# Optimization experiments

Hardware: AMD Instinct MI355X
Metric: run time of the kernel (lower is better)

Reference implementation:

```python
import math
import jax, jax.numpy as jnp
import numpy as np

D_MODEL = 1024
D_HIDDEN = 4096
N_EXPERTS = 8
TOP_K = 2
CAPACITY_FACTOR = 1.25


def setup_inputs() -> dict:
    key = jax.random.key(0)
    ks = jax.random.split(key, 8)
    s = 0.02
    x = jax.random.normal(ks[0], (4, 2048, D_MODEL), dtype=jnp.float32)
    router_w = jax.random.normal(ks[1], (D_MODEL, N_EXPERTS), dtype=jnp.float32) * s
    router_b = jnp.zeros((N_EXPERTS,), dtype=jnp.float32)
    w1 = jax.random.normal(ks[2], (N_EXPERTS, D_MODEL, D_HIDDEN), dtype=jnp.float32) * s
    b1 = jnp.zeros((N_EXPERTS, D_HIDDEN), dtype=jnp.float32)
    w2 = jax.random.normal(ks[3], (N_EXPERTS, D_HIDDEN, D_MODEL), dtype=jnp.float32) * s
    b2 = jnp.zeros((N_EXPERTS, D_MODEL), dtype=jnp.float32)
    return {"x": x, "router_w": router_w, "router_b": router_b,
            "w1": w1, "b1": b1, "w2": w2, "b2": b2}


def reference(x, router_w, router_b, w1, b1, w2, b2):
    B, T, D = x.shape
    N = B * T
    E = N_EXPERTS
    capacity = max(1, math.ceil(N / E * CAPACITY_FACTOR))

    x_flat = x.reshape(N, D)
    # Router (torch casts input to float32 for router)
    logits = x_flat.astype(jnp.float32) @ router_w + router_b          # [N, E]
    gates = jax.nn.softmax(logits, axis=-1)                            # [N, E]

    _, topk_idx = jax.lax.top_k(gates, TOP_K)                          # [N, k]
    expert_mask = jax.nn.one_hot(topk_idx, E, dtype=jnp.int32).sum(1)  # [N, E]

    # Capacity masking via cumulative position per expert
    pos = jnp.cumsum(expert_mask, axis=0) - 1                          # [N, E]
    expert_mask = expert_mask * (pos < capacity)
    valid = expert_mask > 0                                            # [N, E] bool

    # Dispatch: scatter tokens into [E, capacity, D] buffers (invalid -> slot `capacity`)
    pos_c = jnp.where(valid, pos, capacity)                            # [N, E]
    e_idx = jnp.broadcast_to(jnp.arange(E), (N, E))
    dispatched = (x_flat[:, None, :] * valid[:, :, None].astype(x.dtype))
    buf = jnp.zeros((E, capacity + 1, D), x.dtype).at[
        e_idx.ravel(), pos_c.ravel()].add(dispatched.reshape(N * E, D))
    buf = buf[:, :capacity]                                            # [E, C, D]

    # Per-expert FFN as batched GEMMs (GELU exact, matching nn.GELU default)
    h = jax.nn.gelu(jnp.einsum('ecd,edh->ech', buf, w1) + b1[:, None, :],
                    approximate=False)
    out = jnp.einsum('ech,ehd->ecd', h, w2) + b2[:, None, :]           # [E, C, D]

    # Combine: gather each token's expert outputs, weight by raw softmax gate
    pos_g = jnp.minimum(pos_c, capacity - 1)
    gathered = out[e_idx, pos_g]                                       # [N, E, D]
    weights = (gates * valid).astype(x.dtype)                          # [N, E]
    y = jnp.einsum('ned,ne->nd', gathered, weights)
    return y.reshape(B, T, D)
```

## Files before the change

kernel.cpp:

```cpp
#include <hip/hip_runtime.h>
#include <math.h>

#define D_MODEL 1024
#define D_HIDDEN 4096
#define NEXP 8
#define NTOK 8192
#define CAP 1280

#define BM 128
#define BN 128
#define BK 32
#define KSPLIT 2
#define KHALF (D_HIDDEN / KSPLIT)

typedef __attribute__((ext_vector_type(8))) short short8x;
typedef __attribute__((ext_vector_type(4))) short short4x;
typedef __attribute__((ext_vector_type(4))) float float4x;

__device__ __forceinline__ short f2bf(float f) {
  unsigned u = __float_as_uint(f);
  unsigned r = (u + 0x7FFFu + ((u >> 16) & 1u)) >> 16;
  return (short)r;
}
__device__ __forceinline__ float bf2f(short s) {
  return __uint_as_float(((unsigned)(unsigned short)s) << 16);
}
__device__ __forceinline__ float gelu_fast(float v) {
  float u2 = v * (1.5957691216f + 0.0713548163f * v * v);
  return v / (1.0f + __expf(-u2));
}

#define GLDS16(g, l)                                                        \
  __builtin_amdgcn_global_load_lds(                                         \
      (const __attribute__((address_space(1))) void*)(g),                   \
      (__attribute__((address_space(3))) void*)(l), 16, 0, 0)

__global__ __launch_bounds__(256) void convert_x_kernel(
    const float* __restrict__ x, short* __restrict__ xbf) {
  size_t i = ((size_t)blockIdx.x * 256 + threadIdx.x) * 8;
  const float4* s = (const float4*)(x + i);
  float4 a = s[0], b = s[1];
  short8x o;
  o[0] = f2bf(a.x); o[1] = f2bf(a.y); o[2] = f2bf(a.z); o[3] = f2bf(a.w);
  o[4] = f2bf(b.x); o[5] = f2bf(b.y); o[6] = f2bf(b.z); o[7] = f2bf(b.w);
  *(short8x*)(xbf + i) = o;
}

__global__ __launch_bounds__(256) void transpose_kernel(
    const float* __restrict__ in, short* __restrict__ out, int K, int N) {
  __shared__ unsigned tile[32 * 65];
  int n0 = blockIdx.x * 64, k0 = blockIdx.y * 64, e = blockIdx.z;
  int t = threadIdx.x;
  int rr = t >> 4;
  int cc = (t & 15) * 4;
  const float* src = in + (size_t)e * K * N + (size_t)(k0 + rr) * N + n0 + cc;
  bool packer = (rr & 1) == 0;
  int mb = rr >> 1;
#pragma unroll
  for (int p = 0; p < 4; ++p) {
    float4 v = *(const float4*)(src + (size_t)p * 16 * N);
    float4 wv;
    wv.x = __shfl_xor(v.x, 16, 64);
    wv.y = __shfl_xor(v.y, 16, 64);
    wv.z = __shfl_xor(v.z, 16, 64);
    wv.w = __shfl_xor(v.w, 16, 64);
    if (packer) {
      int m = p * 8 + mb;
      unsigned* tr = &tile[m * 65 + cc];
      tr[0] = (unsigned)(unsigned short)f2bf(v.x) |
              ((unsigned)(unsigned short)f2bf(wv.x) << 16);
      tr[1] = (unsigned)(unsigned short)f2bf(v.y) |
              ((unsigned)(unsigned short)f2bf(wv.y) << 16);
      tr[2] = (unsigned)(unsigned short)f2bf(v.z) |
              ((unsigned)(unsigned short)f2bf(wv.z) << 16);
      tr[3] = (unsigned)(unsigned short)f2bf(v.w) |
              ((unsigned)(unsigned short)f2bf(wv.w) << 16);
    }
  }
  __syncthreads();
  int n = t >> 2, q = t & 3;
  const unsigned* col = &tile[q * 8 * 65 + n];
  unsigned d[8];
#pragma unroll
  for (int j = 0; j < 8; ++j) d[j] = col[j * 65];
  short* dst = out + (size_t)e * N * K + (size_t)(n0 + n) * K + k0 + q * 16;
  ((uint4*)dst)[0] = make_uint4(d[0], d[1], d[2], d[3]);
  ((uint4*)dst)[1] = make_uint4(d[4], d[5], d[6], d[7]);
}

__global__ __launch_bounds__(256) void router_kernel(
    const float* __restrict__ x, const float* __restrict__ rw,
    const float* __restrict__ rb, int2* __restrict__ tok_experts,
    float2* __restrict__ tok_gates) {
  int t = blockIdx.x * 4 + (threadIdx.x >> 6);
  int lane = threadIdx.x & 63;
  const float* xr = x + (size_t)t * D_MODEL;
  float acc[8];
#pragma unroll
  for (int e = 0; e < 8; ++e) acc[e] = 0.f;
#pragma unroll
  for (int kk = 0; kk < 16; ++kk) {
    int k = kk * 64 + lane;
    float xv = xr[k];
    const float4* wr = (const float4*)(rw + (size_t)k * 8);
    float4 w0 = wr[0], w1v = wr[1];
    acc[0] += xv * w0.x;  acc[1] += xv * w0.y;
    acc[2] += xv * w0.z;  acc[3] += xv * w0.w;
    acc[4] += xv * w1v.x; acc[5] += xv * w1v.y;
    acc[6] += xv * w1v.z; acc[7] += xv * w1v.w;
  }
#pragma unroll
  for (int off = 32; off > 0; off >>= 1) {
#pragma unroll
    for (int e = 0; e < 8; ++e) acc[e] += __shfl_xor(acc[e], off, 64);
  }
  if (lane == 0) {
    float lg[8];
#pragma unroll
    for (int e = 0; e < 8; ++e) lg[e] = acc[e] + rb[e];
    int e0 = 0;
#pragma unroll
    for (int e = 1; e < 8; ++e) if (lg[e] > lg[e0]) e0 = e;
    int e1 = (e0 == 0) ? 1 : 0;
#pragma unroll
    for (int e = 0; e < 8; ++e) if (e != e0 && lg[e] > lg[e1]) e1 = e;
    float mx = lg[e0];
    float s = 0.f;
#pragma unroll
    for (int e = 0; e < 8; ++e) s += expf(lg[e] - mx);
    float inv = 1.f / s;
    tok_experts[t] = make_int2(e0, e1);
    tok_gates[t] = make_float2(expf(lg[e0] - mx) * inv, expf(lg[e1] - mx) * inv);
  }
}

__global__ __launch_bounds__(1024) void scan_kernel(
    const int2* __restrict__ tok_experts, int* __restrict__ slot_token,
    int* __restrict__ token_rows) {
  int e = blockIdx.x;
  int tid = threadIdx.x;
  for (int i = tid; i < CAP; i += 1024) slot_token[e * CAP + i] = -1;
  __shared__ int wsum[16];
  __shared__ int running;
  if (tid == 0) running = 0;
  __syncthreads();
  int lane = tid & 63, wid = tid >> 6;
  unsigned long long lmask = (1ull << lane) - 1ull;
  for (int base = 0; base < NTOK; base += 1024) {
    int t = base + tid;
    int2 ee = tok_experts[t];
    int m = (ee.x == e || ee.y == e) ? 1 : 0;
    unsigned long long bal = __ballot(m);
    int prefix = __popcll(bal & lmask);
    if (lane == 0) wsum[wid] = (int)__popcll(bal);
    __syncthreads();
    if (tid == 0) {
      int s = running;
#pragma unroll
      for (int w = 0; w < 16; ++w) { int v = wsum[w]; wsum[w] = s; s += v; }
      running = s;
    }
    __syncthreads();
    if (m) {
      int pos = wsum[wid] + prefix;
      int which = (ee.x == e) ? 0 : 1;
      if (pos < CAP) {
        slot_token[e * CAP + pos] = t;
        token_rows[2 * t + which] = e * CAP + pos;
      } else {
        token_rows[2 * t + which] = -1;
      }
    }
    __syncthreads();
  }
}


__global__ __launch_bounds__(256) void gemm1_fast(
    const short* __restrict__ xbf, const short* __restrict__ w1t,
    const float* __restrict__ b1, const int* __restrict__ slot_token,
    short* __restrict__ h) {
  __shared__ short As[BM * BK];
  __shared__ short Bs[BN * BK];
  __shared__ int rowtok[BM];
  int bx = blockIdx.x;
  int e = bx & 7, ct = (bx >> 3) & 31, rt = bx >> 8;
  int tid = threadIdx.x;
  if (tid < BM) {
    int t = slot_token[e * CAP + rt * BM + tid];
    rowtok[tid] = t < 0 ? 0 : t;
  }
  __syncthreads();
  int lane = tid & 63, w = tid >> 6;

  const char* agm[2]; const char* bgm[2];
  char* alds[2]; char* blds[2];
#pragma unroll
  for (int p = 0; p < 2; ++p) {
    int r = w * 32 + p * 16 + (lane >> 2);
    int c = ((lane & 3) - ((r >> 1) & 3)) & 3;
    agm[p] = (const char*)(xbf + (size_t)rowtok[r] * D_MODEL + c * 8);
    alds[p] = (char*)As + (w * 32 + p * 16) * 64 + lane * 16;
    bgm[p] = (const char*)(w1t + ((size_t)e * D_HIDDEN + ct * BN + r) * D_MODEL + c * 8);
    blds[p] = (char*)Bs + (w * 32 + p * 16) * 64 + lane * 16;
  }
  int l15 = lane & 15, q = lane >> 4;
  int swz = (q + ((l15 >> 1) & 3)) & 3;
  const char* afb = (const char*)As + (w * 32 + l15) * 64 + swz * 16;
  const char* bfb = (const char*)Bs + l15 * 64 + swz * 16;

  float4x acc[2][8];
#pragma unroll
  for (int i = 0; i < 2; ++i)
#pragma unroll
    for (int j = 0; j < 8; ++j) acc[i][j] = (float4x){0.f, 0.f, 0.f, 0.f};

  for (int k0 = 0; k0 < D_MODEL; k0 += BK) {
    __syncthreads();
    int kb = k0 * 2;
    GLDS16(agm[0] + kb, alds[0]);
    GLDS16(agm[1] + kb, alds[1]);
    GLDS16(bgm[0] + kb, blds[0]);
    GLDS16(bgm[1] + kb, blds[1]);
    __syncthreads();
    short8x a0 = *(const short8x*)afb;
    short8x a1 = *(const short8x*)(afb + 1024);
#pragma unroll
    for (int j = 0; j < 8; ++j) {
      short8x b = *(const short8x*)(bfb + j * 1024);
      acc[0][j] = __builtin_amdgcn_mfma_f32_16x16x32_bf16(a0, b, acc[0][j], 0, 0, 0);
      acc[1][j] = __builtin_amdgcn_mfma_f32_16x16x32_bf16(a1, b, acc[1][j], 0, 0, 0);
    }
  }
  int col0 = ct * BN;
  int rbase = q * 4;
#pragma unroll
  for (int i = 0; i < 2; ++i) {
#pragma unroll
    for (int j = 0; j < 8; ++j) {
      int col = col0 + j * 16 + l15;
      float bias = b1[e * D_HIDDEN + col];
#pragma unroll
      for (int r = 0; r < 4; ++r) {
        int grow = rt * BM + w * 32 + i * 16 + rbase + r;
        float v = gelu_fast(acc[i][j][r] + bias);
        h[(size_t)(e * CAP + grow) * D_HIDDEN + col] = f2bf(v);
      }
    }
  }
}

__global__ __launch_bounds__(256) void gemm2_fast(
    const short* __restrict__ h, const short* __restrict__ w2t,
    const float* __restrict__ b2, short* __restrict__ p0,
    short* __restrict__ p1) {
  __shared__ short As[BM * BK];
  __shared__ short Bs[BN * BK];
  int bx = blockIdx.x;
  int e = bx & 7;
  int rest = bx >> 3;
  int ct = rest & 7;
  int rg = rest >> 3;
  int rt = rg >> 1, ks = rg & 1;
  int koff = ks * KHALF;
  int tid = threadIdx.x;
  int lane = tid & 63, w = tid >> 6;

  const char* agm[2]; const char* bgm[2];
  char* alds[2]; char* blds[2];
#pragma unroll
  for (int p = 0; p < 2; ++p) {
    int r = w * 32 + p * 16 + (lane >> 2);
    int c = ((lane & 3) - ((r >> 1) & 3)) & 3;
    agm[p] = (const char*)(h + (size_t)(e * CAP + rt * BM + r) * D_HIDDEN + koff + c * 8);
    alds[p] = (char*)As + (w * 32 + p * 16) * 64 + lane * 16;
    bgm[p] = (const char*)(w2t + ((size_t)e * D_MODEL + ct * BN + r) * D_HIDDEN + koff + c * 8);
    blds[p] = (char*)Bs + (w * 32 + p * 16) * 64 + lane * 16;
  }
  int l15 = lane & 15, q = lane >> 4;
  int swz = (q + ((l15 >> 1) & 3)) & 3;
  const char* afb = (const char*)As + (w * 32 + l15) * 64 + swz * 16;
  const char* bfb = (const char*)Bs + l15 * 64 + swz * 16;

  float4x acc[2][8];
#pragma unroll
  for (int i = 0; i < 2; ++i)
#pragma unroll
    for (int j = 0; j < 8; ++j) acc[i][j] = (float4x){0.f, 0.f, 0.f, 0.f};

  for (int k0 = 0; k0 < KHALF; k0 += BK) {
    __syncthreads();
    int kb = k0 * 2;
    GLDS16(agm[0] + kb, alds[0]);
    GLDS16(agm[1] + kb, alds[1]);
    GLDS16(bgm[0] + kb, blds[0]);
    GLDS16(bgm[1] + kb, blds[1]);
    __syncthreads();
    short8x a0 = *(const short8x*)afb;
    short8x a1 = *(const short8x*)(afb + 1024);
#pragma unroll
    for (int j = 0; j < 8; ++j) {
      short8x b = *(const short8x*)(bfb + j * 1024);
      acc[0][j] = __builtin_amdgcn_mfma_f32_16x16x32_bf16(a0, b, acc[0][j], 0, 0, 0);
      acc[1][j] = __builtin_amdgcn_mfma_f32_16x16x32_bf16(a1, b, acc[1][j], 0, 0, 0);
    }
  }
  short* dst = ks == 0 ? p0 : p1;
  int col0 = ct * BN;
  int rbase = q * 4;
#pragma unroll
  for (int i = 0; i < 2; ++i) {
#pragma unroll
    for (int j = 0; j < 8; ++j) {
      int col = col0 + j * 16 + l15;
      float bias = (ks == 0) ? b2[e * D_MODEL + col] : 0.f;
#pragma unroll
      for (int r = 0; r < 4; ++r) {
        int grow = rt * BM + w * 32 + i * 16 + rbase + r;
        float v = acc[i][j][r] + bias;
        dst[(size_t)(e * CAP + grow) * D_MODEL + col] = f2bf(v);
      }
    }
  }
}

__global__ __launch_bounds__(256) void combine_kernel(
    const int* __restrict__ token_rows, const float2* __restrict__ tok_gates,
    const short* __restrict__ p0, const short* __restrict__ p1,
    float* __restrict__ y) {
  int t = blockIdx.x;
  int r0 = token_rows[2 * t], r1 = token_rows[2 * t + 1];
  float2 g = tok_gates[t];
  int d = threadIdx.x * 4;
  float4 v; v.x = v.y = v.z = v.w = 0.f;
  if (r0 >= 0) {
    short4x a = *(const short4x*)(p0 + (size_t)r0 * D_MODEL + d);
    short4x b = *(const short4x*)(p1 + (size_t)r0 * D_MODEL + d);
    v.x += g.x * (bf2f(a[0]) + bf2f(b[0]));
    v.y += g.x * (bf2f(a[1]) + bf2f(b[1]));
    v.z += g.x * (bf2f(a[2]) + bf2f(b[2]));
    v.w += g.x * (bf2f(a[3]) + bf2f(b[3]));
  }
  if (r1 >= 0) {
    short4x a = *(const short4x*)(p0 + (size_t)r1 * D_MODEL + d);
    short4x b = *(const short4x*)(p1 + (size_t)r1 * D_MODEL + d);
    v.x += g.y * (bf2f(a[0]) + bf2f(b[0]));
    v.y += g.y * (bf2f(a[1]) + bf2f(b[1]));
    v.z += g.y * (bf2f(a[2]) + bf2f(b[2]));
    v.w += g.y * (bf2f(a[3]) + bf2f(b[3]));
  }
  *(float4*)(y + (size_t)t * D_MODEL + d) = v;
}

extern "C" void kernel_launch(void* const* d_in, const int* in_sizes, int n_in,
                              void* d_out, int out_size, void* d_ws, size_t ws_size,
                              hipStream_t stream) {
  const float* x  = (const float*)d_in[0];
  const float* rw = (const float*)d_in[1];
  const float* rb = (const float*)d_in[2];
  const float* w1 = (const float*)d_in[3];
  const float* b1 = (const float*)d_in[4];
  const float* w2 = (const float*)d_in[5];
  const float* b2 = (const float*)d_in[6];
  float* y = (float*)d_out;
  (void)in_sizes; (void)n_in; (void)out_size; (void)ws_size;

  char* p = (char*)d_ws;
  size_t off = 0;
  auto take = [&](size_t bytes) -> void* {
    void* r = p + off;
    off = (off + bytes + 255) & ~(size_t)255;
    return r;
  };
  int2*   tok_experts = (int2*)  take((size_t)NTOK * sizeof(int2));
  float2* tok_gates   = (float2*)take((size_t)NTOK * sizeof(float2));
  int*    slot_token  = (int*)   take((size_t)NEXP * CAP * sizeof(int));
  int*    token_rows  = (int*)   take((size_t)NTOK * 2 * sizeof(int));
  short*  xbf         = (short*) take((size_t)NTOK * D_MODEL * sizeof(short));
  short*  w1t         = (short*) take((size_t)NEXP * D_HIDDEN * D_MODEL * sizeof(short));
  short*  w2t         = (short*) take((size_t)NEXP * D_MODEL * D_HIDDEN * sizeof(short));
  short*  h           = (short*) take((size_t)NEXP * CAP * D_HIDDEN * sizeof(short));
  short*  out2        = (short*) take((size_t)NEXP * CAP * D_MODEL * sizeof(short));
  short* part0 = out2;
  short* part1 = w1t;

  router_kernel<<<NTOK / 4, 256, 0, stream>>>(x, rw, rb, tok_experts, tok_gates);
  scan_kernel<<<NEXP, 1024, 0, stream>>>(tok_experts, slot_token, token_rows);
  convert_x_kernel<<<NTOK * D_MODEL / (256 * 8), 256, 0, stream>>>(x, xbf);
  transpose_kernel<<<dim3(D_HIDDEN / 64, D_MODEL / 64, NEXP), 256, 0, stream>>>(
      w1, w1t, D_MODEL, D_HIDDEN);
  transpose_kernel<<<dim3(D_MODEL / 64, D_HIDDEN / 64, NEXP), 256, 0, stream>>>(
      w2, w2t, D_HIDDEN, D_MODEL);
  gemm1_fast<<<2560, 256, 0, stream>>>(xbf, w1t, b1, slot_token, h);
  gemm2_fast<<<1280, 256, 0, stream>>>(h, w2t, b2, part0, part1);
  combine_kernel<<<NTOK, 256, 0, stream>>>(token_rows, tok_gates, part0, part1, y);
}
```

Before: 618.1 us.

## Replace expert GEMMs with 256x256 double-buffered phased MFMA kernel and split-K 4

Replaces the two 128x128 single-buffered expert GEMM kernels with one templated 512-thread kernel. It uses 256x256 tiles, a 128KB double-buffered LDS ring loaded through global_load_lds, and XOR-swizzled fragment reads. Each K step is split into four MFMA phases, with the next tile's loads issued in between, explicit vmcnt/lgkmcnt waits, barriers and setprio around the MFMA bursts. The second GEMM moves to a 4-way K split, which adds two extra partial buffers (reusing the w1t workspace) and two more reads per expert row in combine.

New measurement: 596.5 us. -3.5%, faster.

```diff
diff --git a/kernel.cpp b/kernel.cpp
--- a/kernel.cpp
+++ b/kernel.cpp
@@ -6,12 +6,7 @@
 #define NEXP 8
 #define NTOK 8192
 #define CAP 1280
-
-#define BM 128
-#define BN 128
-#define BK 32
-#define KSPLIT 2
-#define KHALF (D_HIDDEN / KSPLIT)
+#define KSPLIT 4
 
 typedef __attribute__((ext_vector_type(8))) short short8x;
 typedef __attribute__((ext_vector_type(4))) short short4x;
@@ -30,10 +25,11 @@
   return v / (1.0f + __expf(-u2));
 }
 
-#define GLDS16(g, l)                                                        \
-  __builtin_amdgcn_global_load_lds(                                         \
-      (const __attribute__((address_space(1))) void*)(g),                   \
-      (__attribute__((address_space(3))) void*)(l), 16, 0, 0)
+__device__ __forceinline__ void glds16(const void* g, void* l) {
+  __builtin_amdgcn_global_load_lds(
+      (const __attribute__((address_space(1))) void*)g,
+      (__attribute__((address_space(3))) void*)l, 16, 0, 0);
+}
 
 __global__ __launch_bounds__(256) void convert_x_kernel(
     const float* __restrict__ x, short* __restrict__ xbf) {
@@ -176,149 +172,185 @@
 }
 
 
-__global__ __launch_bounds__(256) void gemm1_fast(
-    const short* __restrict__ xbf, const short* __restrict__ w1t,
-    const float* __restrict__ b1, const int* __restrict__ slot_token,
-    short* __restrict__ h) {
-  __shared__ short As[BM * BK];
-  __shared__ short Bs[BN * BK];
-  __shared__ int rowtok[BM];
-  int bx = blockIdx.x;
-  int e = bx & 7, ct = (bx >> 3) & 31, rt = bx >> 8;
-  int tid = threadIdx.x;
-  if (tid < BM) {
-    int t = slot_token[e * CAP + rt * BM + tid];
-    rowtok[tid] = t < 0 ? 0 : t;
-  }
-  __syncthreads();
-  int lane = tid & 63, w = tid >> 6;
-
-  const char* agm[2]; const char* bgm[2];
-  char* alds[2]; char* blds[2];
-#pragma unroll
-  for (int p = 0; p < 2; ++p) {
-    int r = w * 32 + p * 16 + (lane >> 2);
-    int c = ((lane & 3) - ((r >> 1) & 3)) & 3;
-    agm[p] = (const char*)(xbf + (size_t)rowtok[r] * D_MODEL + c * 8);
-    alds[p] = (char*)As + (w * 32 + p * 16) * 64 + lane * 16;
-    bgm[p] = (const char*)(w1t + ((size_t)e * D_HIDDEN + ct * BN + r) * D_MODEL + c * 8);
-    blds[p] = (char*)Bs + (w * 32 + p * 16) * 64 + lane * 16;
-  }
-  int l15 = lane & 15, q = lane >> 4;
-  int swz = (q + ((l15 >> 1) & 3)) & 3;
-  const char* afb = (const char*)As + (w * 32 + l15) * 64 + swz * 16;
-  const char* bfb = (const char*)Bs + l15 * 64 + swz * 16;
-
-  float4x acc[2][8];
-#pragma unroll
-  for (int i = 0; i < 2; ++i)
-#pragma unroll
-    for (int j = 0; j < 8; ++j) acc[i][j] = (float4x){0.f, 0.f, 0.f, 0.f};
-
-  for (int k0 = 0; k0 < D_MODEL; k0 += BK) {
-    __syncthreads();
-    int kb = k0 * 2;
-    GLDS16(agm[0] + kb, alds[0]);
-    GLDS16(agm[1] + kb, alds[1]);
-    GLDS16(bgm[0] + kb, blds[0]);
-    GLDS16(bgm[1] + kb, blds[1]);
-    __syncthreads();
-    short8x a0 = *(const short8x*)afb;
-    short8x a1 = *(const short8x*)(afb + 1024);
-#pragma unroll
-    for (int j = 0; j < 8; ++j) {
-      short8x b = *(const short8x*)(bfb + j * 1024);
-      acc[0][j] = __builtin_amdgcn_mfma_f32_16x16x32_bf16(a0, b, acc[0][j], 0, 0, 0);
-      acc[1][j] = __builtin_amdgcn_mfma_f32_16x16x32_bf16(a1, b, acc[1][j], 0, 0, 0);
-    }
-  }
-  int col0 = ct * BN;
-  int rbase = q * 4;
-#pragma unroll
-  for (int i = 0; i < 2; ++i) {
-#pragma unroll
-    for (int j = 0; j < 8; ++j) {
-      int col = col0 + j * 16 + l15;
-      float bias = b1[e * D_HIDDEN + col];
-#pragma unroll
-      for (int r = 0; r < 4; ++r) {
-        int grow = rt * BM + w * 32 + i * 16 + rbase + r;
-        float v = gelu_fast(acc[i][j][r] + bias);
-        h[(size_t)(e * CAP + grow) * D_HIDDEN + col] = f2bf(v);
-      }
-    }
-  }
-}
-
-__global__ __launch_bounds__(256) void gemm2_fast(
-    const short* __restrict__ h, const short* __restrict__ w2t,
-    const float* __restrict__ b2, short* __restrict__ p0,
-    short* __restrict__ p1) {
-  __shared__ short As[BM * BK];
-  __shared__ short Bs[BN * BK];
+#define BARX() __builtin_amdgcn_s_barrier()
+#define LGKM0()                                      \
+  asm volatile("s_waitcnt lgkmcnt(0)" ::: "memory"); \
+  __builtin_amdgcn_sched_barrier(0)
+#define VMW(n) asm volatile("s_waitcnt vmcnt(" #n ")" ::: "memory")
+
+template <int MODE>
+__global__ __launch_bounds__(512, 2) void gemm_8phase(
+    const short* __restrict__ A, const short* __restrict__ Bw,
+    const float* __restrict__ bias, const int* __restrict__ slot_token,
+    short* __restrict__ o0, short* __restrict__ o1, short* __restrict__ o2,
+    short* __restrict__ o3) {
+  constexpr int NCOL = (MODE == 1) ? D_HIDDEN : D_MODEL;
+  constexpr int ARSH = (MODE == 1) ? D_MODEL : D_HIDDEN;
+  constexpr int BRSH = (MODE == 1) ? D_MODEL : D_HIDDEN;
+  constexpr int NT = 16;
+
+  __shared__ __align__(1024) char lds[131072];
+
   int bx = blockIdx.x;
   int e = bx & 7;
   int rest = bx >> 3;
-  int ct = rest & 7;
-  int rg = rest >> 3;
-  int rt = rg >> 1, ks = rg & 1;
-  int koff = ks * KHALF;
+  int rt = rest % 5;
+  int c2 = rest / 5;
+  int ct, ks;
+  if constexpr (MODE == 1) { ct = c2; ks = 0; }
+  else { ct = c2 & 3; ks = c2 >> 2; }
+
   int tid = threadIdx.x;
-  int lane = tid & 63, w = tid >> 6;
-
-  const char* agm[2]; const char* bgm[2];
-  char* alds[2]; char* blds[2];
-#pragma unroll
-  for (int p = 0; p < 2; ++p) {
-    int r = w * 32 + p * 16 + (lane >> 2);
-    int c = ((lane & 3) - ((r >> 1) & 3)) & 3;
-    agm[p] = (const char*)(h + (size_t)(e * CAP + rt * BM + r) * D_HIDDEN + koff + c * 8);
-    alds[p] = (char*)As + (w * 32 + p * 16) * 64 + lane * 16;
-    bgm[p] = (const char*)(w2t + ((size_t)e * D_MODEL + ct * BN + r) * D_HIDDEN + koff + c * 8);
-    blds[p] = (char*)Bs + (w * 32 + p * 16) * 64 + lane * 16;
-  }
-  int l15 = lane & 15, q = lane >> 4;
-  int swz = (q + ((l15 >> 1) & 3)) & 3;
-  const char* afb = (const char*)As + (w * 32 + l15) * 64 + swz * 16;
-  const char* bfb = (const char*)Bs + l15 * 64 + swz * 16;
-
-  float4x acc[2][8];
-#pragma unroll
-  for (int i = 0; i < 2; ++i)
-#pragma unroll
-    for (int j = 0; j < 8; ++j) acc[i][j] = (float4x){0.f, 0.f, 0.f, 0.f};
-
-  for (int k0 = 0; k0 < KHALF; k0 += BK) {
-    __syncthreads();
-    int kb = k0 * 2;
-    GLDS16(agm[0] + kb, alds[0]);
-    GLDS16(agm[1] + kb, alds[1]);
-    GLDS16(bgm[0] + kb, blds[0]);
-    GLDS16(bgm[1] + kb, blds[1]);
-    __syncthreads();
-    short8x a0 = *(const short8x*)afb;
-    short8x a1 = *(const short8x*)(afb + 1024);
-#pragma unroll
-    for (int j = 0; j < 8; ++j) {
-      short8x b = *(const short8x*)(bfb + j * 1024);
-      acc[0][j] = __builtin_amdgcn_mfma_f32_16x16x32_bf16(a0, b, acc[0][j], 0, 0, 0);
-      acc[1][j] = __builtin_amdgcn_mfma_f32_16x16x32_bf16(a1, b, acc[1][j], 0, 0, 0);
-    }
-  }
-  short* dst = ks == 0 ? p0 : p1;
-  int col0 = ct * BN;
-  int rbase = q * 4;
-#pragma unroll
-  for (int i = 0; i < 2; ++i) {
-#pragma unroll
-    for (int j = 0; j < 8; ++j) {
-      int col = col0 + j * 16 + l15;
-      float bias = (ks == 0) ? b2[e * D_MODEL + col] : 0.f;
-#pragma unroll
-      for (int r = 0; r < 4; ++r) {
-        int grow = rt * BM + w * 32 + i * 16 + rbase + r;
-        float v = acc[i][j][r] + bias;
-        dst[(size_t)(e * CAP + grow) * D_MODEL + col] = f2bf(v);
+  int w = tid >> 6, l = tid & 63;
+  int wr = w >> 2, wc = w & 3;
+
+  int cg16 = (((l & 7) ^ ((l >> 3) & 7)) << 4);
+  size_t koff = (size_t)ks * (D_HIDDEN / KSPLIT) * 2;
+
+  const char* ast[4];
+  const char* bst[4];
+#pragma unroll
+  for (int h = 0; h < 2; ++h) {
+#pragma unroll
+    for (int i = 0; i < 2; ++i) {
+      int r = h * 128 + i * 64 + w * 8 + (l >> 3);
+      int p = h * 2 + i;
+      if constexpr (MODE == 1) {
+        int t = slot_token[e * CAP + rt * 256 + r];
+        if (t < 0) t = 0;
+        ast[p] = (const char*)A + (size_t)t * (ARSH * 2) + cg16;
+      } else {
+        ast[p] = (const char*)A + (size_t)(e * CAP + rt * 256 + r) * (ARSH * 2) +
+                 koff + cg16;
+      }
+      bst[p] = (const char*)Bw + (size_t)(e * NCOL + ct * 256 + r) * (BRSH * 2) +
+               koff + cg16;
+    }
+  }
+  char* ldsb = (char*)lds;
+  int wofs = w * 1024;
+
+#define STG_(stg, matoff, h, ktB, buf)                                         \
+  glds16(stg[(h) * 2 + 0] + (ktB),                                             \
+         ldsb + (buf) * 65536 + (matoff) + (h) * 16384 + wofs);                \
+  glds16(stg[(h) * 2 + 1] + (ktB),                                             \
+         ldsb + (buf) * 65536 + (matoff) + (h) * 16384 + 8192 + wofs)
+#define STG_A(h, ktB, buf) STG_(ast, 0, h, ktB, buf)
+#define STG_B(h, ktB, buf) STG_(bst, 32768, h, ktB, buf)
+
+  int lane_row = (l & 15) * 128;
+  int ck0 = ((((l >> 4) + 0) ^ (l & 7)) << 4);
+  int ck1 = ((((l >> 4) + 4) ^ (l & 7)) << 4);
+
+  short8x av[4][2], bv[2][2];
+  float4x acc[8][4];
+#pragma unroll
+  for (int m = 0; m < 8; ++m)
+#pragma unroll
+    for (int n = 0; n < 4; ++n) acc[m][n] = (float4x){0.f, 0.f, 0.f, 0.f};
+
+#define LDA_(Mq, cur)                                                          \
+  {                                                                            \
+    const char* ap_ =                                                          \
+        ldsb + (cur) * 65536 + wr * 16384 + (Mq) * 8192 + lane_row;            \
+    av[0][0] = *(const short8x*)(ap_ + 0 * 2048 + ck0);                        \
+    av[0][1] = *(const short8x*)(ap_ + 0 * 2048 + ck1);                        \
+    av[1][0] = *(const short8x*)(ap_ + 1 * 2048 + ck0);                        \
+    av[1][1] = *(const short8x*)(ap_ + 1 * 2048 + ck1);                        \
+    av[2][0] = *(const short8x*)(ap_ + 2 * 2048 + ck0);                        \
+    av[2][1] = *(const short8x*)(ap_ + 2 * 2048 + ck1);                        \
+    av[3][0] = *(const short8x*)(ap_ + 3 * 2048 + ck0);                        \
+    av[3][1] = *(const short8x*)(ap_ + 3 * 2048 + ck1);                        \
+  }
+#define LDB_(Nq, cur)                                                          \
+  {                                                                            \
+    const char* bp_ = ldsb + (cur) * 65536 + 32768 + wc * 8192 +               \
+                      (Nq) * 4096 + lane_row;                                  \
+    bv[0][0] = *(const short8x*)(bp_ + 0 * 2048 + ck0);                        \
+    bv[0][1] = *(const short8x*)(bp_ + 0 * 2048 + ck1);                        \
+    bv[1][0] = *(const short8x*)(bp_ + 1 * 2048 + ck0);                        \
+    bv[1][1] = *(const short8x*)(bp_ + 1 * 2048 + ck1);                        \
+  }
+#define MFMA16(Mq, Nq)                                                         \
+  __builtin_amdgcn_s_setprio(1);                                               \
+  _Pragma("unroll") for (int mm = 0; mm < 4; ++mm) {                           \
+    _Pragma("unroll") for (int nn = 0; nn < 2; ++nn) {                         \
+      float4x* ac = &acc[(Mq) * 4 + mm][(Nq) * 2 + nn];                        \
+      *ac = __builtin_amdgcn_mfma_f32_16x16x32_bf16(av[mm][0], bv[nn][0], *ac, \
+                                                    0, 0, 0);                  \
+      *ac = __builtin_amdgcn_mfma_f32_16x16x32_bf16(av[mm][1], bv[nn][1], *ac, \
+                                                    0, 0, 0);                  \
+    }                                                                          \
+  }                                                                            \
+  __builtin_amdgcn_s_setprio(0)
+
+  STG_A(0, 0, 0);
+  STG_B(0, 0, 0);
+  STG_A(1, 0, 0);
+  STG_B(1, 0, 0);
+  STG_A(0, 128, 1);
+  STG_B(0, 128, 1);
+  VMW(4);
+  BARX();
+
+#define KBODY(uu, cur, nxt)                                                    \
+  {                                                                            \
+    int kb1 = ((uu) + 1) * 128, kb2 = ((uu) + 2) * 128;                        \
+                                                                      \
+    LDA_(0, cur); LDB_(0, cur);                                                \
+    if ((uu) + 1 < NT) { STG_A(1, kb1, nxt); }                                 \
+    BARX(); LGKM0(); MFMA16(0, 0); BARX();                                     \
+                                                                      \
+    LDB_(1, cur);                                                              \
+    if ((uu) + 1 < NT) { STG_B(1, kb1, nxt); }                                 \
+    BARX(); LGKM0(); MFMA16(0, 1); BARX();                                     \
+                                                                      \
+    LDA_(1, cur); LDB_(0, cur);                                                \
+    if ((uu) + 2 < NT) { STG_A(0, kb2, cur); }                                 \
+    BARX(); LGKM0(); MFMA16(1, 0); BARX();                                     \
+                                                                      \
+    LDB_(1, cur);                                                              \
+    if ((uu) + 2 < NT) { STG_B(0, kb2, cur); }                                 \
+    if ((uu) < NT - 2) { VMW(4); } else { VMW(0); }                            \
+    BARX(); LGKM0(); MFMA16(1, 1); BARX();                                     \
+  }
+
+#pragma unroll 1
+  for (int u = 0; u < NT; u += 2) {
+    KBODY(u, 0, 1);
+    KBODY(u + 1, 1, 0);
+  }
+
+  int q4 = (l >> 4) * 4, l15 = l & 15;
+  if constexpr (MODE == 1) {
+#pragma unroll
+    for (int m = 0; m < 8; ++m) {
+      int grow = rt * 256 + wr * 128 + m * 16 + q4;
+      size_t rowb = (size_t)(e * CAP + grow) * NCOL;
+#pragma unroll
+      for (int n = 0; n < 4; ++n) {
+        int col = ct * 256 + wc * 64 + n * 16 + l15;
+        float bs = bias[e * NCOL + col];
+#pragma unroll
+        for (int r = 0; r < 4; ++r) {
+          float v = gelu_fast(acc[m][n][r] + bs);
+          o0[rowb + (size_t)r * NCOL + col] = f2bf(v);
+        }
+      }
+    }
+  } else {
+    short* dst = (ks == 0) ? o0 : (ks == 1) ? o1 : (ks == 2) ? o2 : o3;
+#pragma unroll
+    for (int m = 0; m < 8; ++m) {
+      int grow = rt * 256 + wr * 128 + m * 16 + q4;
+      size_t rowb = (size_t)(e * CAP + grow) * NCOL;
+#pragma unroll
+      for (int n = 0; n < 4; ++n) {
+        int col = ct * 256 + wc * 64 + n * 16 + l15;
+        float bs = (ks == 0) ? bias[e * NCOL + col] : 0.f;
+#pragma unroll
+        for (int r = 0; r < 4; ++r)
+          dst[rowb + (size_t)r * NCOL + col] = f2bf(acc[m][n][r] + bs);
       }
     }
   }
@@ -327,6 +359,7 @@
 __global__ __launch_bounds__(256) void combine_kernel(
     const int* __restrict__ token_rows, const float2* __restrict__ tok_gates,
     const short* __restrict__ p0, const short* __restrict__ p1,
+    const short* __restrict__ p2, const short* __restrict__ p3,
     float* __restrict__ y) {
   int t = blockIdx.x;
   int r0 = token_rows[2 * t], r1 = token_rows[2 * t + 1];
@@ -334,20 +367,26 @@
   int d = threadIdx.x * 4;
   float4 v; v.x = v.y = v.z = v.w = 0.f;
   if (r0 >= 0) {
-    short4x a = *(const short4x*)(p0 + (size_t)r0 * D_MODEL + d);
-    short4x b = *(const short4x*)(p1 + (size_t)r0 * D_MODEL + d);
-    v.x += g.x * (bf2f(a[0]) + bf2f(b[0]));
-    v.y += g.x * (bf2f(a[1]) + bf2f(b[1]));
-    v.z += g.x * (bf2f(a[2]) + bf2f(b[2]));
-    v.w += g.x * (bf2f(a[3]) + bf2f(b[3]));
+    size_t b = (size_t)r0 * D_MODEL + d;
+    short4x a0 = *(const short4x*)(p0 + b);
+    short4x a1 = *(const short4x*)(p1 + b);
+    short4x a2 = *(const short4x*)(p2 + b);
+    short4x a3 = *(const short4x*)(p3 + b);
+    v.x += g.x * (bf2f(a0[0]) + bf2f(a1[0]) + bf2f(a2[0]) + bf2f(a3[0]));
+    v.y += g.x * (bf2f(a0[1]) + bf2f(a1[1]) + bf2f(a2[1]) + bf2f(a3[1]));
+    v.z += g.x * (bf2f(a0[2]) + bf2f(a1[2]) + bf2f(a2[2]) + bf2f(a3[2]));
+    v.w += g.x * (bf2f(a0[3]) + bf2f(a1[3]) + bf2f(a2[3]) + bf2f(a3[3]));
   }
   if (r1 >= 0) {
-    short4x a = *(const short4x*)(p0 + (size_t)r1 * D_MODEL + d);
-    short4x b = *(const short4x*)(p1 + (size_t)r1 * D_MODEL + d);
-    v.x += g.y * (bf2f(a[0]) + bf2f(b[0]));
-    v.y += g.y * (bf2f(a[1]) + bf2f(b[1]));
-    v.z += g.y * (bf2f(a[2]) + bf2f(b[2]));
-    v.w += g.y * (bf2f(a[3]) + bf2f(b[3]));
+    size_t b = (size_t)r1 * D_MODEL + d;
+    short4x a0 = *(const short4x*)(p0 + b);
+    short4x a1 = *(const short4x*)(p1 + b);
+    short4x a2 = *(const short4x*)(p2 + b);
+    short4x a3 = *(const short4x*)(p3 + b);
+    v.x += g.y * (bf2f(a0[0]) + bf2f(a1[0]) + bf2f(a2[0]) + bf2f(a3[0]));
+    v.y += g.y * (bf2f(a0[1]) + bf2f(a1[1]) + bf2f(a2[1]) + bf2f(a3[1]));
+    v.z += g.y * (bf2f(a0[2]) + bf2f(a1[2]) + bf2f(a2[2]) + bf2f(a3[2]));
+    v.w += g.y * (bf2f(a0[3]) + bf2f(a1[3]) + bf2f(a2[3]) + bf2f(a3[3]));
   }
   *(float4*)(y + (size_t)t * D_MODEL + d) = v;
 }
@@ -383,6 +422,8 @@
   short*  out2        = (short*) take((size_t)NEXP * CAP * D_MODEL * sizeof(short));
   short* part0 = out2;
   short* part1 = w1t;
+  short* part2 = w1t + (size_t)NEXP * CAP * D_MODEL;
+  short* part3 = w1t + (size_t)2 * NEXP * CAP * D_MODEL;
 
   router_kernel<<<NTOK / 4, 256, 0, stream>>>(x, rw, rb, tok_experts, tok_gates);
   scan_kernel<<<NEXP, 1024, 0, stream>>>(tok_experts, slot_token, token_rows);
@@ -391,7 +432,10 @@
       w1, w1t, D_MODEL, D_HIDDEN);
   transpose_kernel<<<dim3(D_MODEL / 64, D_HIDDEN / 64, NEXP), 256, 0, stream>>>(
       w2, w2t, D_HIDDEN, D_MODEL);
-  gemm1_fast<<<2560, 256, 0, stream>>>(xbf, w1t, b1, slot_token, h);
-  gemm2_fast<<<1280, 256, 0, stream>>>(h, w2t, b2, part0, part1);
-  combine_kernel<<<NTOK, 256, 0, stream>>>(token_rows, tok_gates, part0, part1, y);
-}
+  gemm_8phase<1><<<640, 512, 0, stream>>>(xbf, w1t, b1, slot_token, h,
+                                          nullptr, nullptr, nullptr);
+  gemm_8phase<2><<<640, 512, 0, stream>>>(h, w2t, b2, nullptr, part0, part1,
+                                          part2, part3);
+  combine_kernel<<<NTOK, 256, 0, stream>>>(token_rows, tok_gates, part0, part1,
+                                           part2, part3, y);
+}
```
